# Kernel optimization log

Measured on AMD Instinct MI355X. Metric: run time of the kernel, lower is better.

Reference implementation:

```python
import jax, jax.numpy as jnp
import numpy as np

N, E = 100000, 1600000
F_IN, H, K, C = 165, 128, 3, 2


def _norm_weights(edge_index, n):
    # PyG ChebConv.__norm__ with normalization='sym', lambda_max=2.0:
    # remove self loops, deg from row, w = -D^-1/2 A D^-1/2 off-diag, diag = 0.
    src, dst = edge_index[0], edge_index[1]
    mask = (src != dst).astype(jnp.float32)
    deg = jax.ops.segment_sum(mask, src, num_segments=n)
    dinv = jnp.where(deg > 0, jax.lax.rsqrt(jnp.where(deg > 0, deg, 1.0)), 0.0)
    return -dinv[src] * dinv[dst] * mask  # [E]


def _cheb_conv(x, W, b, src, dst, w, n):
    # Chebyshev recurrence: Tx0 = x, Tx1 = Lhat x, Tx_k = 2 Lhat Tx_{k-1} - Tx_{k-2}
    def prop(h):  # sparse Lhat @ h via gather + segment_sum
        return jax.ops.segment_sum(w[:, None] * h[src], dst, num_segments=n)

    out = x @ W[0]
    Tx0, Tx1 = x, prop(x)
    out = out + Tx1 @ W[1]
    for k in range(2, W.shape[0]):
        Tx2 = 2.0 * prop(Tx1) - Tx0
        out = out + Tx2 @ W[k]
        Tx0, Tx1 = Tx1, Tx2
    return out + b


def setup_inputs() -> dict:
    key = jax.random.key(0)
    ks = jax.random.split(key, 8)
    x = jax.random.normal(ks[0], (N, F_IN), dtype=jnp.float32)
    edge_index = jax.random.randint(ks[1], (2, E), 0, N, dtype=jnp.int64)
    s1 = 1.0 / np.sqrt(F_IN)
    s2 = 1.0 / np.sqrt(H)
    W1 = jax.random.uniform(ks[2], (K, F_IN, H), jnp.float32, -s1, s1)
    b1 = jnp.zeros((H,), jnp.float32)
    W2 = jax.random.uniform(ks[3], (K, H, H), jnp.float32, -s2, s2)
    b2 = jnp.zeros((H,), jnp.float32)
    Wl = jax.random.uniform(ks[4], (H, C), jnp.float32, -s2, s2)
    bl = jax.random.uniform(ks[5], (C,), jnp.float32, -s2, s2)
    return {"x": x, "edge_index": edge_index, "W1": W1, "b1": b1,
            "W2": W2, "b2": b2, "Wl": Wl, "bl": bl}


def reference(x, edge_index, W1, b1, W2, b2, Wl, bl):
    n = x.shape[0]
    src, dst = edge_index[0], edge_index[1]
    w = _norm_weights(edge_index, n)
    h = jax.nn.relu(_cheb_conv(x, W1, b1, src, dst, w, n))
    # F.dropout(training=self.training) is identity in eval mode
    h = h + _cheb_conv(h, W2, b2, src, dst, w, n)  # residual skip
    logits = jax.nn.log_softmax(h @ Wl + bl, axis=-1)
    return (logits, edge_index)
```

## Files before the change

kernel.cpp:

```cpp
#include <hip/hip_runtime.h>
#include <stdint.h>

typedef __bf16 bf16;
typedef unsigned char u8;
typedef __attribute__((ext_vector_type(8))) __bf16 bf16x8;
typedef __attribute__((ext_vector_type(4))) float f32x4;
typedef __attribute__((ext_vector_type(2))) float f32x2;

#define N_NODES 100000
#define F_IN 165
#define NB 391
#define NBLK 320

static inline int cdiv(int a, int b) { return (a + b - 1) / b; }

__device__ __forceinline__ float bfu(unsigned hw) {
  union { unsigned u; float f; } v; v.u = hw << 16; return v.f;
}
__device__ __forceinline__ unsigned packbf2(float a, float b) {
  bf16 x = (bf16)a, y = (bf16)b;
  unsigned short sx = __builtin_bit_cast(unsigned short, x);
  unsigned short sy = __builtin_bit_cast(unsigned short, y);
  return (unsigned)sx | ((unsigned)sy << 16);
}
__device__ __forceinline__ u8 f32_to_fp8(float v) {
  int t = __builtin_amdgcn_cvt_pk_fp8_f32(v, 0.f, 0, false);
  return (u8)(t & 0xff);
}

__device__ __forceinline__ void async16(const bf16* g, const bf16* l) {
  __builtin_amdgcn_global_load_lds(
      (const __attribute__((address_space(1))) void*)g,
      (__attribute__((address_space(3))) void*)l, 16, 0, 0);
}

__global__ void detect_k(const int* __restrict__ ei32, int* __restrict__ flag) {
  int i = blockIdx.x * 256 + threadIdx.x;
  int v = ei32[2 * i + 1];
  if (v != 0) atomicOr(flag, 1);
}


__global__ __launch_bounds__(256) void hist_k(const int* __restrict__ ei, int E,
                                              const int* __restrict__ flag,
                                              int* __restrict__ gcd, int* __restrict__ gcs) {
  __shared__ int hd[NB], hs[NB];
  int b = blockIdx.x, t = threadIdx.x;
  for (int i = t; i < NB; i += 256) { hd[i] = 0; hs[i] = 0; }
  __syncthreads();
  int sh = (*flag) ? 0 : 1;
  int CH = (E + NBLK - 1) / NBLK;
  int lo = b * CH, hi = min(E, lo + CH);
  for (int e = lo + t; e < hi; e += 256) {
    int s = ei[(size_t)e << sh];
    int d = ei[(size_t)(E + e) << sh];
    if ((unsigned)s < (unsigned)N_NODES && (unsigned)d < (unsigned)N_NODES && s != d) {
      atomicAdd(&hd[d >> 8], 1);
      atomicAdd(&hs[s >> 8], 1);
    }
  }
  __syncthreads();
  for (int i = t; i < NB; i += 256) {
    gcd[i * NBLK + b] = hd[i];
    gcs[i * NBLK + b] = hs[i];
  }
}

__global__ __launch_bounds__(256) void scat2_k(const int* __restrict__ ei, int E,
                                               const int* __restrict__ flag,
                                               const int* __restrict__ ofd,
                                               const int* __restrict__ ofs,
                                               unsigned* __restrict__ pkAll) {
  __shared__ int based[NB], bases[NB];
  int b = blockIdx.x, t = threadIdx.x;
  for (int i = t; i < NB; i += 256) {
    based[i] = ofd[i * NBLK + b];
    bases[i] = ofs[i * NBLK + b];
  }
  __syncthreads();
  int sh = (*flag) ? 0 : 1;
  int CH = (E + NBLK - 1) / NBLK;
  int lo = b * CH, hi = min(E, lo + CH);
  for (int e = lo + t; e < hi; e += 256) {
    int s = ei[(size_t)e << sh];
    int d = ei[(size_t)(E + e) << sh];
    if ((unsigned)s < (unsigned)N_NODES && (unsigned)d < (unsigned)N_NODES && s != d) {
      int pd = atomicAdd(&based[d >> 8], 1);
      pkAll[pd] = ((unsigned)(d & 255) << 24) | (unsigned)s;
      int ps = atomicAdd(&bases[s >> 8], 1);
      pkAll[ps] = (unsigned)s;
    }
  }
}

__global__ __launch_bounds__(256) void fin_dst_k(const unsigned* __restrict__ pk,
                                                 const int* __restrict__ ofd,
                                                 const int* __restrict__ totald,
                                                 int* __restrict__ rowptr,
                                                 int* __restrict__ csr) {
  __shared__ int fh[256], fb[256];
  int b = blockIdx.x, t = threadIdx.x;
  int lo = ofd[b * NBLK];
  int hi = (b == NB - 1) ? *totald : ofd[(b + 1) * NBLK];
  fh[t] = 0;
  __syncthreads();
  for (int i = lo + t; i < hi; i += 256) atomicAdd(&fh[pk[i] >> 24], 1);
  __syncthreads();
  fb[t] = fh[t];
  __syncthreads();
  for (int offv = 1; offv < 256; offv <<= 1) {
    int x = (t >= offv) ? fb[t - offv] : 0;
    __syncthreads();
    fb[t] += x;
    __syncthreads();
  }
  int excl = fb[t] - fh[t];
  int node = b * 256 + t;
  if (node <= N_NODES) rowptr[node] = lo + excl;
  __syncthreads();
  fb[t] = lo + excl;
  __syncthreads();
  for (int i = lo + t; i < hi; i += 256) {
    unsigned v = pk[i];
    int pos = atomicAdd(&fb[v >> 24], 1);
    csr[pos] = (int)(v & 0xFFFFFFu);
  }
}

__global__ __launch_bounds__(256) void fin_src_k(const unsigned* __restrict__ pk,
                                                 const int* __restrict__ ofs,
                                                 const int* __restrict__ grand,
                                                 float* __restrict__ dinv) {
  __shared__ int fh[256];
  int b = blockIdx.x, t = threadIdx.x;
  int lo = ofs[b * NBLK];
  int hi = (b == NB - 1) ? *grand : ofs[(b + 1) * NBLK];
  fh[t] = 0;
  __syncthreads();
  for (int i = lo + t; i < hi; i += 256) atomicAdd(&fh[pk[i] & 255], 1);
  __syncthreads();
  int node = b * 256 + t;
  if (node < N_NODES) {
    int dg = fh[t];
    dinv[node] = dg > 0 ? rsqrtf((float)dg) : 0.f;
  }
}


__global__ void scanA_k(const int* __restrict__ cnt, int* __restrict__ bsum, int nElem) {
  __shared__ int s[256];
  int b = blockIdx.x, t = threadIdx.x;
  int base = b * 1024;
  int sum = 0;
  for (int i = t; i < 1024; i += 256) {
    int idx = base + i;
    sum += (idx < nElem) ? cnt[idx] : 0;
  }
  s[t] = sum; __syncthreads();
  for (int off = 128; off > 0; off >>= 1) {
    if (t < off) s[t] += s[t + off];
    __syncthreads();
  }
  if (t == 0) bsum[b] = s[0];
}

__global__ void scanB_k(int* __restrict__ bsum, int* __restrict__ totalOut, int nChunk) {
  __shared__ int s[256];
  int t = threadIdx.x;
  int v = (t < nChunk) ? bsum[t] : 0;
  s[t] = v; __syncthreads();
  for (int off = 1; off < 256; off <<= 1) {
    int x = (t >= off) ? s[t - off] : 0;
    __syncthreads();
    s[t] += x;
    __syncthreads();
  }
  int excl = s[t] - v;
  if (t < nChunk) bsum[t] = excl;
  if (t == 255) *totalOut = s[255];
}

__global__ void scanC_k(const int* __restrict__ cnt, const int* __restrict__ bsum,
                        int* __restrict__ outp, int nElem) {
  __shared__ int s[256];
  int b = blockIdx.x, t = threadIdx.x;
  int base = b * 1024 + t * 4;
  int v[4]; int tot = 0;
  for (int i = 0; i < 4; i++) {
    int idx = base + i;
    v[i] = (idx < nElem) ? cnt[idx] : 0;
    tot += v[i];
  }
  s[t] = tot; __syncthreads();
  for (int off = 1; off < 256; off <<= 1) {
    int x = (t >= off) ? s[t - off] : 0;
    __syncthreads();
    s[t] += x;
    __syncthreads();
  }
  int excl = s[t] - tot + bsum[b];
  for (int i = 0; i < 4; i++) {
    int idx = base + i;
    if (idx < nElem) { outp[idx] = excl; excl += v[i]; }
  }
}


__global__ void build_wct_k(const float* __restrict__ W, bf16* __restrict__ out, int Fin, int Kp) {
  int idx = blockIdx.x * 256 + threadIdx.x;
  if (idx >= 384 * Kp) return;
  int r = idx / Kp, k = idx % Kp;
  int t = r >> 7, j = r & 127;
  float v = 0.f;
  if (k < Fin) {
    if (t == 0)
      v = W[(size_t)k * 128 + j] - W[(size_t)2 * Fin * 128 + (size_t)k * 128 + j];
    else if (t == 1)
      v = W[(size_t)Fin * 128 + (size_t)k * 128 + j];
    else
      v = 2.f * W[(size_t)2 * Fin * 128 + (size_t)k * 128 + j];
  }
  out[(size_t)r * Kp + k] = (bf16)v;
}

__global__ void prep_k(const float* __restrict__ W2, const float* __restrict__ Wl,
                       const float* __restrict__ b2, const float* __restrict__ bl,
                       float* __restrict__ wlc, float* __restrict__ cc,
                       u8* __restrict__ g0, u8* __restrict__ g1) {
  int t = threadIdx.x;
  if (t < 16) ((unsigned*)(g0 + (size_t)N_NODES * 64))[t] = 0;
  else if (t < 32) ((unsigned*)(g1 + (size_t)N_NODES * 64))[t - 16] = 0;
  if (t < 128) {
    int f = t;
    float c00 = 0, c01 = 0, c10 = 0, c11 = 0, c20 = 0, c21 = 0;
    for (int k = 0; k < 128; k++) {
      float w0 = W2[(size_t)f * 128 + k];
      float w1 = W2[(size_t)128 * 128 + f * 128 + k];
      float w2 = W2[(size_t)2 * 128 * 128 + f * 128 + k];
      float l0 = Wl[k * 2], l1 = Wl[k * 2 + 1];
      c00 += (w0 - w2) * l0; c01 += (w0 - w2) * l1;
      c10 += w1 * l0;        c11 += w1 * l1;
      c20 += 2.f * w2 * l0;  c21 += 2.f * w2 * l1;
    }
    c00 += Wl[f * 2]; c01 += Wl[f * 2 + 1];
    wlc[0 * 128 + f] = c00; wlc[1 * 128 + f] = c01;
    wlc[2 * 128 + f] = c10; wlc[3 * 128 + f] = c11;
    wlc[4 * 128 + f] = c20; wlc[5 * 128 + f] = c21;
  } else if (t < 192) {
    int c = t - 128;
    float p0 = b2[2 * c] * Wl[(2 * c) * 2] + b2[2 * c + 1] * Wl[(2 * c + 1) * 2];
    float p1 = b2[2 * c] * Wl[(2 * c) * 2 + 1] + b2[2 * c + 1] * Wl[(2 * c + 1) * 2 + 1];
#pragma unroll
    for (int off = 32; off > 0; off >>= 1) {
      p0 += __shfl_down(p0, off);
      p1 += __shfl_down(p1, off);
    }
    if (c == 0) { cc[0] = p0 + bl[0]; cc[1] = p1 + bl[1]; }
  }
}

__global__ void pad_x_k(const float* __restrict__ x, bf16* __restrict__ xp) {
  int idx = blockIdx.x * 256 + threadIdx.x;
  if (idx >= N_NODES * 96) return;
  int n = idx / 96, k = (idx % 96) * 2;
  float a = (k < F_IN) ? x[(size_t)n * F_IN + k] : 0.f;
  float b = (k + 1 < F_IN) ? x[(size_t)n * F_IN + k + 1] : 0.f;
  *(unsigned*)(xp + (size_t)n * 192 + k) = packbf2(a, b);
}


__global__ __launch_bounds__(256) void gemm3_k(const bf16* __restrict__ A, int lda,
                                               const bf16* __restrict__ Bt, int K,
                                               bf16* __restrict__ C0, bf16* __restrict__ C1,
                                               u8* __restrict__ C2g,
                                               const float* __restrict__ dinv, int M) {
  __shared__ __align__(16) bf16 As[128 * 32];
  __shared__ __align__(16) bf16 Bs[128 * 32];
  const int tid = threadIdx.x;
  const int w = tid >> 6, l = tid & 63;
  const int mBase = blockIdx.x * 128;
  const int nb = blockIdx.y * 128;
  const int wm = (w >> 1) * 64, wn = (w & 1) * 64;
  const int lr = l & 15, lq = l >> 4;
  f32x4 acc[4][4] = {};
  for (int k0 = 0; k0 < K; k0 += 32) {
#pragma unroll
    for (int p = 0; p < 2; ++p) {
      int q = w * 2 + p;
      int row = q * 16 + (l >> 2);
      int seg = (l & 3) * 8;
      int ar = mBase + row; if (ar > M - 1) ar = M - 1;
      async16(A + (size_t)ar * lda + k0 + seg, &As[q * 512]);
      async16(Bt + (size_t)(nb + row) * K + k0 + seg, &Bs[q * 512]);
    }
    __syncthreads();
    bf16x8 a[4], b[4];
#pragma unroll
    for (int i = 0; i < 4; i++) a[i] = *(const bf16x8*)&As[(wm + i * 16 + lr) * 32 + lq * 8];
#pragma unroll
    for (int j = 0; j < 4; j++) b[j] = *(const bf16x8*)&Bs[(wn + j * 16 + lr) * 32 + lq * 8];
#pragma unroll
    for (int i = 0; i < 4; i++)
#pragma unroll
      for (int j = 0; j < 4; j++)
        acc[i][j] = __builtin_amdgcn_mfma_f32_16x16x32_bf16(a[i], b[j], acc[i][j], 0, 0, 0);
    __syncthreads();
  }
  if (blockIdx.y == 2) {
#pragma unroll
    for (int i = 0; i < 4; i++) {
#pragma unroll
      for (int r = 0; r < 4; r++) {
        int row = mBase + wm + i * 16 + lq * 4 + r;
        if (row < M) {
          float dv = dinv[row];
#pragma unroll
          for (int j = 0; j < 4; j++) {
            int col = wn + j * 16 + lr;
            C2g[(size_t)row * 128 + col] = f32_to_fp8(dv * acc[i][j][r]);
          }
        }
      }
    }
  } else {
    bf16* __restrict__ C = blockIdx.y ? C1 : C0;
#pragma unroll
    for (int i = 0; i < 4; i++) {
#pragma unroll
      for (int r = 0; r < 4; r++) {
        int row = mBase + wm + i * 16 + lq * 4 + r;
        if (row < M) {
#pragma unroll
          for (int j = 0; j < 4; j++) {
            int col = wn + j * 16 + lr;
            C[(size_t)row * 128 + col] = (bf16)acc[i][j][r];
          }
        }
      }
    }
  }
}

__global__ void cvt48_k(const u8* __restrict__ g8, u8* __restrict__ g4) {
  int i = blockIdx.x * 256 + threadIdx.x;
  if (i >= N_NODES * 16) return;
  int n = i >> 4, j = i & 15;
  uint2 w = *(const uint2*)(g8 + (size_t)n * 128 + j * 8);
  auto a0 = __builtin_amdgcn_cvt_pk_f32_fp8((int)w.x, false);
  auto a1 = __builtin_amdgcn_cvt_pk_f32_fp8((int)w.x, true);
  auto a2 = __builtin_amdgcn_cvt_pk_f32_fp8((int)w.y, false);
  auto a3 = __builtin_amdgcn_cvt_pk_f32_fp8((int)w.y, true);
  unsigned u = 0;
  u = __builtin_amdgcn_cvt_scalef32_pk_fp4_f32(u, 2.f * a0[0], 2.f * a0[1], 1.f, 0);
  u = __builtin_amdgcn_cvt_scalef32_pk_fp4_f32(u, 2.f * a1[0], 2.f * a1[1], 1.f, 1);
  u = __builtin_amdgcn_cvt_scalef32_pk_fp4_f32(u, 2.f * a2[0], 2.f * a2[1], 1.f, 2);
  u = __builtin_amdgcn_cvt_scalef32_pk_fp4_f32(u, 2.f * a3[0], 2.f * a3[1], 1.f, 3);
  *(unsigned*)(g4 + (size_t)n * 64 + j * 4) = u;
}

template <int MODE>
__global__ __launch_bounds__(256) void prop_k(const int* __restrict__ rowptr,
                                              const int* __restrict__ csr,
                                              const u8* __restrict__ g4,
                                              const float* __restrict__ dinv,
                                              const bf16* __restrict__ addA,
                                              const float* __restrict__ bias,
                                              const float* __restrict__ wlc,
                                              u8* __restrict__ out4,
                                              f32x2* __restrict__ V0,
                                              f32x2* __restrict__ V1,
                                              f32x2* __restrict__ V2s) {
  const int n = blockIdx.x * 4 + (threadIdx.x >> 6);
  const int lane = threadIdx.x & 63;
  const int qq = lane >> 4, j = lane & 15;
  const int beg = rowptr[n], end = rowptr[n + 1];
  const unsigned jb = (unsigned)j << 2;

  const float dn = dinv[n];
  uint4 ua = *(const uint4*)(addA + (size_t)n * 128 + j * 8);
  f32x4 bq0, bq1;
  if (MODE == 1) {
    bq0 = *(const f32x4*)(bias + 8 * j);
    bq1 = *(const f32x4*)(bias + 8 * j + 4);
  }

  f32x2 av[4] = {};

  int c[8];
#pragma unroll
  for (int u = 0; u < 8; u++) {
    int iu = beg + 4 * u + qq;
    c[u] = (iu < end) ? csr[iu] : N_NODES;
  }
  for (int e0 = beg; e0 < end; e0 += 32) {
    unsigned w[8];
#pragma unroll
    for (int u = 0; u < 8; u++)
      w[u] = *(const unsigned*)(g4 + (((unsigned)c[u] << 6) | jb));
#pragma unroll
    for (int u = 0; u < 8; u++) {
      int iu = e0 + 32 + 4 * u + qq;
      c[u] = (iu < end) ? csr[iu] : N_NODES;
    }
#pragma unroll
    for (int u = 0; u < 8; u++) {
      av[0] += __builtin_amdgcn_cvt_scalef32_pk_f32_fp4(w[u], 1.f, 0);
      av[1] += __builtin_amdgcn_cvt_scalef32_pk_f32_fp4(w[u], 1.f, 1);
      av[2] += __builtin_amdgcn_cvt_scalef32_pk_f32_fp4(w[u], 1.f, 2);
      av[3] += __builtin_amdgcn_cvt_scalef32_pk_f32_fp4(w[u], 1.f, 3);
    }
  }
#pragma unroll
  for (int off = 32; off >= 16; off >>= 1) {
#pragma unroll
    for (int k = 0; k < 4; k++) {
      av[k].x += __shfl_down(av[k].x, off);
      av[k].y += __shfl_down(av[k].y, off);
    }
  }

  f32x2 yv[4];
  yv[0].x = bfu(ua.x & 0xffffu); yv[0].y = bfu(ua.x >> 16);
  yv[1].x = bfu(ua.y & 0xffffu); yv[1].y = bfu(ua.y >> 16);
  yv[2].x = bfu(ua.z & 0xffffu); yv[2].y = bfu(ua.z >> 16);
  yv[3].x = bfu(ua.w & 0xffffu); yv[3].y = bfu(ua.w >> 16);

  if (MODE == 0) {
    if (qq == 0) {
      const float m1 = -dn * dn, m2 = 2.f * dn;
      f32x2 ov[4];
#pragma unroll
      for (int k = 0; k < 4; k++) ov[k] = av[k] * m1 + yv[k] * m2;
      unsigned u = 0;
      u = __builtin_amdgcn_cvt_scalef32_pk_fp4_f32(u, ov[0].x, ov[0].y, 1.f, 0);
      u = __builtin_amdgcn_cvt_scalef32_pk_fp4_f32(u, ov[1].x, ov[1].y, 1.f, 1);
      u = __builtin_amdgcn_cvt_scalef32_pk_fp4_f32(u, ov[2].x, ov[2].y, 1.f, 2);
      u = __builtin_amdgcn_cvt_scalef32_pk_fp4_f32(u, ov[3].x, ov[3].y, 1.f, 3);
      *(unsigned*)(out4 + (size_t)n * 64 + j * 4) = u;
    }
  } else {
    const float s = -0.5f * dn;
    f32x2 hv[4];
#pragma unroll
    for (int k = 0; k < 4; k++) {
      f32x2 t = av[k] * s + yv[k];
      f32x2 bb; bb.x = bq0[0], bb.y = bq0[1];
      if (k == 1) { bb.x = bq0[2]; bb.y = bq0[3]; }
      if (k == 2) { bb.x = bq1[0]; bb.y = bq1[1]; }
      if (k == 3) { bb.x = bq1[2]; bb.y = bq1[3]; }
      t += bb;
      hv[k].x = fmaxf(t.x, 0.f);
      hv[k].y = fmaxf(t.y, 0.f);
    }
    float p[6];
#pragma unroll
    for (int c2 = 0; c2 < 6; c2++) {
      f32x4 wa = *(const f32x4*)(wlc + c2 * 128 + 8 * j);
      f32x4 wb = *(const f32x4*)(wlc + c2 * 128 + 8 * j + 4);
      f32x2 w0; w0.x = wa[0]; w0.y = wa[1];
      f32x2 w1; w1.x = wa[2]; w1.y = wa[3];
      f32x2 w2; w2.x = wb[0]; w2.y = wb[1];
      f32x2 w3; w3.x = wb[2]; w3.y = wb[3];
      f32x2 acc = hv[0] * w0;
      acc += hv[1] * w1;
      acc += hv[2] * w2;
      acc += hv[3] * w3;
      p[c2] = acc.x + acc.y;
    }
#pragma unroll
    for (int off = 8; off >= 1; off >>= 1)
#pragma unroll
      for (int c2 = 0; c2 < 6; c2++) p[c2] += __shfl_down(p[c2], off);
    if (lane == 0) {
      f32x2 v0, v1, v2;
      v0.x = p[0]; v0.y = p[1];
      v1.x = p[2]; v1.y = p[3];
      v2.x = dn * p[4]; v2.y = dn * p[5];
      V0[n] = v0; V1[n] = v1; V2s[n] = v2;
    }
  }
}

template <int MODE>
__global__ __launch_bounds__(256) void propT_k(const int* __restrict__ rowptr,
                                               const int* __restrict__ csr,
                                               const f32x2* __restrict__ gsrc,
                                               const float* __restrict__ dinv,
                                               const f32x2* __restrict__ addv,
                                               const float* __restrict__ cc,
                                               f32x2* __restrict__ outv,
                                               float* __restrict__ fout) {
  int n = blockIdx.x * 4 + (threadIdx.x >> 6);
  int l = threadIdx.x & 63;
  int beg = rowptr[n], end = rowptr[n + 1];
  float s0 = 0.f, s1 = 0.f;
  for (int idx = beg + l; idx < end; idx += 64) {
    f32x2 v = gsrc[csr[idx]];
    s0 += v.x;
    s1 += v.y;
  }
#pragma unroll
  for (int off = 32; off > 0; off >>= 1) {
    s0 += __shfl_down(s0, off);
    s1 += __shfl_down(s1, off);
  }
  if (l != 0) return;
  float dn = dinv[n];
  f32x2 av = addv[n];
  if (MODE == 0) {
    f32x2 t;
    t.x = dn * (-dn * s0 + av.x);
    t.y = dn * (-dn * s1 + av.y);
    outv[n] = t;
  } else {
    float z0 = -dn * s0 + av.x + cc[0];
    float z1 = -dn * s1 + av.y + cc[1];
    float m = fmaxf(z0, z1);
    float lse = m + logf(expf(z0 - m) + expf(z1 - m));
    fout[(size_t)n * 2 + 0] = z0 - lse;
    fout[(size_t)n * 2 + 1] = z1 - lse;
  }
}

__global__ void copy_edges_k(const int* __restrict__ ei, const int* __restrict__ flag,
                             float* __restrict__ out, int n) {
  int i = blockIdx.x * 256 + threadIdx.x;
  if (i >= n) return;
  int sh = (*flag) ? 0 : 1;
  out[i] = (float)ei[(size_t)i << sh];
}


extern "C" void kernel_launch(void* const* d_in, const int* in_sizes, int n_in,
                              void* d_out, int out_size, void* d_ws, size_t ws_size,
                              hipStream_t stream) {
  const float* x = (const float*)d_in[0];
  const int* ei = (const int*)d_in[1];
  const float* W1 = (const float*)d_in[2];
  const float* b1 = (const float*)d_in[3];
  const float* W2 = (const float*)d_in[4];
  const float* b2 = (const float*)d_in[5];
  const float* Wl = (const float*)d_in[6];
  const float* bl = (const float*)d_in[7];
  float* outp = (float*)d_out;

  const int N = N_NODES;
  const int E = in_sizes[1] / 2;
  const int L = NB * NBLK;
  const int L2 = 2 * L;
  const int nChunkS = cdiv(L2, 1024);

  char* ws = (char*)d_ws;
  size_t off = 0;
  auto alloc = [&](size_t bytes) {
    off = (off + 255) & ~(size_t)255;
    size_t o = off;
    off += bytes;
    return o;
  };
  int* flag = (int*)(ws + alloc(4));
  int* gcAll = (int*)(ws + alloc((size_t)L2 * 4));
  int* bsum = (int*)(ws + alloc(1024));
  int* grand = (int*)(ws + alloc(4));
  int* rowptr = (int*)(ws + alloc((size_t)(N + 1) * 4));
  float* dinv = (float*)(ws + alloc((size_t)N * 4));
  unsigned* pkAll = (unsigned*)(ws + alloc((size_t)2 * E * 4));
  int* csr = (int*)(ws + alloc((size_t)E * 4));
  bf16* wct1 = (bf16*)(ws + alloc((size_t)384 * 192 * 2));
  float* wlc = (float*)(ws + alloc((size_t)128 * 6 * 4));
  float* cc = (float*)(ws + alloc(8));
  bf16* xp = (bf16*)(ws + alloc((size_t)N * 192 * 2));
  bf16* U0 = (bf16*)(ws + alloc((size_t)N * 128 * 2));
  bf16* U1 = (bf16*)(ws + alloc((size_t)N * 128 * 2));
  u8* G8 = (u8*)(ws + alloc((size_t)N * 128));
  u8* G0 = (u8*)(ws + alloc((size_t)(N + 1) * 64));
  u8* G1 = (u8*)(ws + alloc((size_t)(N + 1) * 64));
  f32x2* V0 = (f32x2*)(ws + alloc((size_t)N * 8));
  f32x2* V1 = (f32x2*)(ws + alloc((size_t)N * 8));
  f32x2* V2s = (f32x2*)(ws + alloc((size_t)N * 8));
  f32x2* tW = (f32x2*)(ws + alloc((size_t)N * 8));
  (void)ws_size;

  int* gcd = gcAll;
  int* gcs = gcAll + L;

  hipMemsetAsync(flag, 0, 4, stream);
  detect_k<<<256, 256, 0, stream>>>(ei, flag);

  hist_k<<<NBLK, 256, 0, stream>>>(ei, E, flag, gcd, gcs);
  scanA_k<<<nChunkS, 256, 0, stream>>>(gcAll, bsum, L2);
  scanB_k<<<1, 256, 0, stream>>>(bsum, grand, nChunkS);
  scanC_k<<<nChunkS, 256, 0, stream>>>(gcAll, bsum, gcAll, L2);
  scat2_k<<<NBLK, 256, 0, stream>>>(ei, E, flag, gcd, gcs, pkAll);
  fin_dst_k<<<NB, 256, 0, stream>>>(pkAll, gcd, gcAll + L, rowptr, csr);
  fin_src_k<<<NB, 256, 0, stream>>>(pkAll, gcs, grand, dinv);

  prep_k<<<1, 256, 0, stream>>>(W2, Wl, b2, bl, wlc, cc, G0, G1);
  pad_x_k<<<cdiv(N * 96, 256), 256, 0, stream>>>(x, xp);
  build_wct_k<<<cdiv(384 * 192, 256), 256, 0, stream>>>(W1, wct1, F_IN, 192);

  const int gm = cdiv(N, 128);
  gemm3_k<<<dim3(gm, 3), 256, 0, stream>>>(xp, 192, wct1, 192, U0, U1, G8, dinv, N);
  cvt48_k<<<cdiv(N * 16, 256), 256, 0, stream>>>(G8, G0);
  prop_k<0><<<N / 4, 256, 0, stream>>>(rowptr, csr, G0, dinv, U1, nullptr, nullptr,
                                       G1, nullptr, nullptr, nullptr);
  prop_k<1><<<N / 4, 256, 0, stream>>>(rowptr, csr, G1, dinv, U0, b1, wlc,
                                       nullptr, V0, V1, V2s);
  propT_k<0><<<N / 4, 256, 0, stream>>>(rowptr, csr, V2s, dinv, V1, nullptr, tW, nullptr);
  propT_k<1><<<N / 4, 256, 0, stream>>>(rowptr, csr, tW, dinv, V0, cc, nullptr, outp);

  copy_edges_k<<<cdiv(2 * E, 256), 256, 0, stream>>>(ei, flag, outp + (size_t)2 * N, 2 * E);
}
```

Before: 436.4 us.

## Fuse edge copy into scatter, remap GEMM blocks per XCD, narrow propT groups

Writes the float edge_index output from inside the scatter kernel, which already reads every edge, and removes the separate copy kernel and its second pass over the edges. Flattens the GEMM grid to 1D and remaps block IDs so that the three column tiles of each row tile land on the same XCD, which should improve L2 reuse of A. Narrows the propT per-node reduction from 64 lanes to 16, since the average degree is about 16, so fewer lanes sit idle. The block remap pads the grid to a multiple of 8 and returns early for the extra blocks.

```diff
diff --git a/kernel.cpp b/kernel.cpp
--- a/kernel.cpp
+++ b/kernel.cpp
@@ -70,7 +70,8 @@
                                                const int* __restrict__ flag,
                                                const int* __restrict__ ofd,
                                                const int* __restrict__ ofs,
-                                               unsigned* __restrict__ pkAll) {
+                                               unsigned* __restrict__ pkAll,
+                                               float* __restrict__ eout) {
   __shared__ int based[NB], bases[NB];
   int b = blockIdx.x, t = threadIdx.x;
   for (int i = t; i < NB; i += 256) {
@@ -84,6 +85,8 @@
   for (int e = lo + t; e < hi; e += 256) {
     int s = ei[(size_t)e << sh];
     int d = ei[(size_t)(E + e) << sh];
+    eout[e] = (float)s;
+    eout[E + e] = (float)d;
     if ((unsigned)s < (unsigned)N_NODES && (unsigned)d < (unsigned)N_NODES && s != d) {
       int pd = atomicAdd(&based[d >> 8], 1);
       pkAll[pd] = ((unsigned)(d & 255) << 24) | (unsigned)s;
@@ -276,10 +279,16 @@
                                                const float* __restrict__ dinv, int M) {
   __shared__ __align__(16) bf16 As[128 * 32];
   __shared__ __align__(16) bf16 Bs[128 * 32];
+  const int b = blockIdx.x;
+  const int xcd = b & 7, kk = b >> 3;
+  const int y = kk % 3;
+  const int m = xcd + 8 * (kk / 3);
+  const int gmv = (M + 127) >> 7;
+  if (m >= gmv) return;
   const int tid = threadIdx.x;
   const int w = tid >> 6, l = tid & 63;
-  const int mBase = blockIdx.x * 128;
-  const int nb = blockIdx.y * 128;
+  const int mBase = m * 128;
+  const int nb = y * 128;
   const int wm = (w >> 1) * 64, wn = (w & 1) * 64;
   const int lr = l & 15, lq = l >> 4;
   f32x4 acc[4][4] = {};
@@ -294,19 +303,19 @@
       async16(Bt + (size_t)(nb + row) * K + k0 + seg, &Bs[q * 512]);
     }
     __syncthreads();
-    bf16x8 a[4], b[4];
+    bf16x8 a[4], bb[4];
 #pragma unroll
     for (int i = 0; i < 4; i++) a[i] = *(const bf16x8*)&As[(wm + i * 16 + lr) * 32 + lq * 8];
 #pragma unroll
-    for (int j = 0; j < 4; j++) b[j] = *(const bf16x8*)&Bs[(wn + j * 16 + lr) * 32 + lq * 8];
+    for (int j = 0; j < 4; j++) bb[j] = *(const bf16x8*)&Bs[(wn + j * 16 + lr) * 32 + lq * 8];
 #pragma unroll
     for (int i = 0; i < 4; i++)
 #pragma unroll
       for (int j = 0; j < 4; j++)
-        acc[i][j] = __builtin_amdgcn_mfma_f32_16x16x32_bf16(a[i], b[j], acc[i][j], 0, 0, 0);
-    __syncthreads();
-  }
-  if (blockIdx.y == 2) {
+        acc[i][j] = __builtin_amdgcn_mfma_f32_16x16x32_bf16(a[i], bb[j], acc[i][j], 0, 0, 0);
+    __syncthreads();
+  }
+  if (y == 2) {
 #pragma unroll
     for (int i = 0; i < 4; i++) {
 #pragma unroll
@@ -323,7 +332,7 @@
       }
     }
   } else {
-    bf16* __restrict__ C = blockIdx.y ? C1 : C0;
+    bf16* __restrict__ C = y ? C1 : C0;
 #pragma unroll
     for (int i = 0; i < 4; i++) {
 #pragma unroll
@@ -490,17 +499,17 @@
                                                const float* __restrict__ cc,
                                                f32x2* __restrict__ outv,
                                                float* __restrict__ fout) {
-  int n = blockIdx.x * 4 + (threadIdx.x >> 6);
-  int l = threadIdx.x & 63;
+  int n = blockIdx.x * 16 + (threadIdx.x >> 4);
+  int l = threadIdx.x & 15;
   int beg = rowptr[n], end = rowptr[n + 1];
   float s0 = 0.f, s1 = 0.f;
-  for (int idx = beg + l; idx < end; idx += 64) {
+  for (int idx = beg + l; idx < end; idx += 16) {
     f32x2 v = gsrc[csr[idx]];
     s0 += v.x;
     s1 += v.y;
   }
 #pragma unroll
-  for (int off = 32; off > 0; off >>= 1) {
+  for (int off = 8; off > 0; off >>= 1) {
     s0 += __shfl_down(s0, off);
     s1 += __shfl_down(s1, off);
   }
@@ -520,14 +529,6 @@
     fout[(size_t)n * 2 + 0] = z0 - lse;
     fout[(size_t)n * 2 + 1] = z1 - lse;
   }
-}
-
-__global__ void copy_edges_k(const int* __restrict__ ei, const int* __restrict__ flag,
-                             float* __restrict__ out, int n) {
-  int i = blockIdx.x * 256 + threadIdx.x;
-  if (i >= n) return;
-  int sh = (*flag) ? 0 : 1;
-  out[i] = (float)ei[(size_t)i << sh];
 }
 
 
@@ -591,7 +592,8 @@
   scanA_k<<<nChunkS, 256, 0, stream>>>(gcAll, bsum, L2);
   scanB_k<<<1, 256, 0, stream>>>(bsum, grand, nChunkS);
   scanC_k<<<nChunkS, 256, 0, stream>>>(gcAll, bsum, gcAll, L2);
-  scat2_k<<<NBLK, 256, 0, stream>>>(ei, E, flag, gcd, gcs, pkAll);
+  scat2_k<<<NBLK, 256, 0, stream>>>(ei, E, flag, gcd, gcs, pkAll,
+                                    outp + (size_t)2 * N);
   fin_dst_k<<<NB, 256, 0, stream>>>(pkAll, gcd, gcAll + L, rowptr, csr);
   fin_src_k<<<NB, 256, 0, stream>>>(pkAll, gcs, grand, dinv);
 
@@ -600,14 +602,13 @@
   build_wct_k<<<cdiv(384 * 192, 256), 256, 0, stream>>>(W1, wct1, F_IN, 192);
 
   const int gm = cdiv(N, 128);
-  gemm3_k<<<dim3(gm, 3), 256, 0, stream>>>(xp, 192, wct1, 192, U0, U1, G8, dinv, N);
+  const int gmp = cdiv(gm, 8) * 8;
+  gemm3_k<<<gmp * 3, 256, 0, stream>>>(xp, 192, wct1, 192, U0, U1, G8, dinv, N);
   cvt48_k<<<cdiv(N * 16, 256), 256, 0, stream>>>(G8, G0);
   prop_k<0><<<N / 4, 256, 0, stream>>>(rowptr, csr, G0, dinv, U1, nullptr, nullptr,
                                        G1, nullptr, nullptr, nullptr);
   prop_k<1><<<N / 4, 256, 0, stream>>>(rowptr, csr, G1, dinv, U0, b1, wlc,
                                        nullptr, V0, V1, V2s);
-  propT_k<0><<<N / 4, 256, 0, stream>>>(rowptr, csr, V2s, dinv, V1, nullptr, tW, nullptr);
-  propT_k<1><<<N / 4, 256, 0, stream>>>(rowptr, csr, tW, dinv, V0, cc, nullptr, outp);
-
-  copy_edges_k<<<cdiv(2 * E, 256), 256, 0, stream>>>(ei, flag, outp + (size_t)2 * N, 2 * E);
-}
+  propT_k<0><<<N / 16, 256, 0, stream>>>(rowptr, csr, V2s, dinv, V1, nullptr, tW, nullptr);
+  propT_k<1><<<N / 16, 256, 0, stream>>>(rowptr, csr, tW, dinv, V0, cc, nullptr, outp);
+}
```

Result: faster. 403.5 us (-7.5%).
